# Optimization experiments

Measured on AMD Instinct MI355X. Metric: run time of the kernel, lower is better.

## Reference

```python
import jax, jax.numpy as jnp
import numpy as np

HEADS = 8
DIM_HEAD = 64
SCALE = DIM_HEAD ** -0.5


def setup_inputs() -> dict:
    key = jax.random.key(0)
    ks = jax.random.split(key, 6)
    b, n, t, d, cond_dim, hidden = 2, 8, 1024, 512, 512, HEADS * DIM_HEAD
    return {
        "x": jax.random.normal(ks[0], (b * n, t, d), dtype=jnp.float32),
        "label_emb_mm": jax.random.normal(ks[1], (b, n, cond_dim), dtype=jnp.float32),
        "Wqkv": jax.random.normal(ks[2], (d, 3 * hidden), dtype=jnp.float32) * (d ** -0.5),
        "Wk": jax.random.normal(ks[3], (cond_dim, hidden), dtype=jnp.float32) * (cond_dim ** -0.5),
        "Wv": jax.random.normal(ks[4], (cond_dim, hidden), dtype=jnp.float32) * (cond_dim ** -0.5),
        "Wout": jax.random.normal(ks[5], (hidden, d), dtype=jnp.float32) * (hidden ** -0.5),
        "b": 2,
    }


def reference(x, label_emb_mm, Wqkv, Wk, Wv, Wout, b):
    bn, t, d = x.shape
    n = bn // b
    h, dh = HEADS, DIM_HEAD
    xb = x.reshape(b, n, t, d)
    # fused QKV projection: (b, n, t, 3*h*dh)
    qkv = xb @ Wqkv
    q, k, v = jnp.split(qkv, 3, axis=-1)

    def to_heads(z):  # (b, n, t, h*dh) -> (b, n, h, t, dh)
        return z.reshape(b, n, t, h, dh).transpose(0, 1, 3, 2, 4)

    q, k, v = to_heads(q), to_heads(k), to_heads(v)
    # per-frame conditioning K/V: one extra token per frame
    ek = (label_emb_mm @ Wk).reshape(b, n, 1, h, dh).transpose(0, 1, 3, 2, 4)
    ev = (label_emb_mm @ Wv).reshape(b, n, 1, h, dh).transpose(0, 1, 3, 2, 4)
    k = jnp.concatenate([ek, k], axis=-2)  # (b, n, h, 1+t, dh)
    v = jnp.concatenate([ev, v], axis=-2)
    q = q * SCALE
    sim = jnp.einsum("bnhid,bnhjd->bnhij", q, k)
    attn = jax.nn.softmax(sim, axis=-1)
    out = jnp.einsum("bnhij,bnhjd->bnhid", attn, v)
    out = out.transpose(0, 1, 3, 2, 4).reshape(b, n, t, h * dh)
    out = out @ Wout
    return out.reshape(b * n, t, d)
```

## Files before the change

kernel.cpp:

```cpp
#include <hip/hip_runtime.h>
#include <stdint.h>

typedef unsigned short u16;
typedef __bf16 bf16x8 __attribute__((ext_vector_type(8)));
typedef float f32x4 __attribute__((ext_vector_type(4)));
typedef float f32x16 __attribute__((ext_vector_type(16)));

__device__ __forceinline__ u16 f2bf(float f) {
  uint32_t u = __builtin_bit_cast(uint32_t, f);
  u += 0x7FFFu + ((u >> 16) & 1u);
  return (u16)(u >> 16);
}
__device__ __forceinline__ float bf2f(u16 v) {
  return __builtin_bit_cast(float, ((uint32_t)v) << 16);
}

#if __has_builtin(__builtin_amdgcn_exp2f)
__device__ __forceinline__ float exp2_fast(float x) { return __builtin_amdgcn_exp2f(x); }
#else
__device__ __forceinline__ float exp2_fast(float x) { return exp2f(x); }
#endif

__device__ __forceinline__ void gload_lds16(const u16* g, u16* l) {
  __builtin_amdgcn_global_load_lds(
      (const __attribute__((address_space(1))) uint32_t*)g,
      (__attribute__((address_space(3))) uint32_t*)l, 16, 0, 0);
}

__device__ __forceinline__ uint32_t cvtpk(float lo, float hi) {
  uint32_t r;
  asm("v_cvt_pk_bf16_f32 %0, %1, %2" : "=v"(r) : "v"(lo), "v"(hi));
  return r;
}
__device__ __forceinline__ void plswap(uint32_t& a, uint32_t& b) {
  asm volatile("v_permlane32_swap_b32 %0, %1" : "+v"(a), "+v"(b));
}

__global__ __launch_bounds__(256) void prep_kernel(
    const float* __restrict__ x, const float* __restrict__ Wqkv,
    const float* __restrict__ Wout, const float* __restrict__ label,
    const float* __restrict__ Wk, const float* __restrict__ Wv,
    u16* __restrict__ xb, u16* __restrict__ WqkvT, u16* __restrict__ WoutT,
    u16* __restrict__ ek, u16* __restrict__ ev, float qscale) {
  const int b = blockIdx.x;
  if (b < 4096) {
    int i = (b * 256 + threadIdx.x) * 8;
    float4 a = *(const float4*)(x + i);
    float4 c = *(const float4*)(x + i + 4);
    union { u16 u[8]; uint4 v; } r;
    r.u[0] = f2bf(a.x); r.u[1] = f2bf(a.y); r.u[2] = f2bf(a.z); r.u[3] = f2bf(a.w);
    r.u[4] = f2bf(c.x); r.u[5] = f2bf(c.y); r.u[6] = f2bf(c.z); r.u[7] = f2bf(c.w);
    *(uint4*)(xb + i) = r.v;
  } else if (b < 7168) {
    int id = (b - 4096) * 256 + threadIdx.x;
    int k = id & 511, nn = id >> 9;
    float v = Wqkv[(size_t)k * 1536 + nn];
    if (nn < 512) v *= qscale;
    WqkvT[id] = f2bf(v);
  } else if (b < 8192) {
    int id = (b - 7168) * 256 + threadIdx.x;
    int k = id & 511, nn = id >> 9;
    WoutT[id] = f2bf(Wout[(size_t)k * 512 + nn]);
  } else {
    __shared__ float sdata[256];
    const int bb = b - 8192;
    const int chunk = bb & 7, row = (bb >> 3) & 15;
    const float* W = (bb & 128) ? Wv : Wk;
    u16* o = (bb & 128) ? ev : ek;
    const int tid = threadIdx.x;
    const int col = chunk * 64 + (tid & 63);
    const int ks = tid >> 6;
    const float* lr = label + row * 512 + ks * 128;
    const float* wp = W + (size_t)(ks * 128) * 512 + col;
    float acc = 0.f;
#pragma unroll 8
    for (int i = 0; i < 128; ++i)
      acc = fmaf(lr[i], wp[(size_t)i * 512], acc);
    sdata[tid] = acc;
    __syncthreads();
    if (tid < 64) {
      float t = sdata[tid] + sdata[tid + 64] + sdata[tid + 128] + sdata[tid + 192];
      o[row * 512 + chunk * 64 + tid] = f2bf(t);
    }
  }
}

template <int MODE>
__global__ __launch_bounds__(512, 2) void gemm_bt_kernel(
    const u16* __restrict__ A, const u16* __restrict__ B,
    u16* __restrict__ OQ, u16* __restrict__ OKb, u16* __restrict__ OVT,
    float* __restrict__ OF, int K, int N) {
  __shared__ __align__(16) u16 As[3][128 * 64];
  __shared__ __align__(16) u16 Bs[3][256 * 64];
  const int tid = threadIdx.x;
  const int w = tid >> 6, lane = tid & 63;
  const int l15 = lane & 15, lg = lane >> 4;
  const int wr = w >> 2, wc = w & 3;

  constexpr int NBY = (MODE == 0) ? 6 : 2;
  const int q8 = gridDim.x >> 3;
  const int cf = blockIdx.x;
  const int wg = (cf & 7) * q8 + (cf >> 3);
  const int bx = wg / NBY, by = wg % NBY;

  const int srow = tid >> 3, schunk = tid & 7;
  const u16* Ag = A + (size_t)(bx * 128 + srow) * K + ((schunk ^ (srow & 7)) * 8);
  const u16* Bg = B + (size_t)(by * 256 + srow) * K + ((schunk ^ (srow & 7)) * 8);

  f32x4 acc[4][4] = {};

  const int nt = K >> 6;
#define STAGE(buf, k0)                                                      \
  {                                                                         \
    gload_lds16(Ag + (k0), &As[buf][(w * 8) * 64]);                         \
    gload_lds16(Ag + (k0) + (size_t)64 * K, &As[buf][(64 + w * 8) * 64]);   \
    _Pragma("unroll") for (int r = 0; r < 4; ++r)                           \
        gload_lds16(Bg + (k0) + (size_t)(r * 64) * K,                       \
                    &Bs[buf][(r * 64 + w * 8) * 64]);                       \
  }
#define COMPUTE(cb)                                                               \
  {                                                                               \
    const u16* Ab = &As[cb][0];                                                   \
    const u16* Bb = &Bs[cb][0];                                                   \
    bf16x8 a[4][2], b[4][2];                                                      \
    _Pragma("unroll") for (int mi = 0; mi < 4; ++mi) {                            \
      const int row = wr * 64 + mi * 16 + l15;                                    \
      _Pragma("unroll") for (int ks = 0; ks < 2; ++ks)                            \
          a[mi][ks] = *(const bf16x8*)&Ab[row * 64 + (((ks * 4 + lg) ^ (row & 7)) * 8)]; \
    }                                                                             \
    _Pragma("unroll") for (int ni = 0; ni < 4; ++ni) {                            \
      const int row = wc * 64 + ni * 16 + l15;                                    \
      _Pragma("unroll") for (int ks = 0; ks < 2; ++ks)                            \
          b[ni][ks] = *(const bf16x8*)&Bb[row * 64 + (((ks * 4 + lg) ^ (row & 7)) * 8)]; \
    }                                                                             \
    __builtin_amdgcn_s_setprio(1);                                                \
    _Pragma("unroll") for (int ks = 0; ks < 2; ++ks)                              \
        _Pragma("unroll") for (int mi = 0; mi < 4; ++mi)                          \
            _Pragma("unroll") for (int ni = 0; ni < 4; ++ni)                      \
                acc[mi][ni] = __builtin_amdgcn_mfma_f32_16x16x32_bf16(             \
                    a[mi][ks], b[ni][ks], acc[mi][ni], 0, 0, 0);                  \
    __builtin_amdgcn_s_setprio(0);                                                \
  }

  STAGE(0, 0);
  STAGE(1, 64);

  int cr = 0, cw = 2;
  for (int t = 0; t < nt - 1; ++t) {
    asm volatile("s_waitcnt vmcnt(6)" ::: "memory");
    __builtin_amdgcn_s_barrier();
    __builtin_amdgcn_sched_barrier(0);
    if (t + 2 < nt) STAGE(cw, (t + 2) * 64);
    COMPUTE(cr);
    cr = (cr == 2) ? 0 : cr + 1;
    cw = (cw == 2) ? 0 : cw + 1;
  }
  asm volatile("s_waitcnt vmcnt(0)" ::: "memory");
  __builtin_amdgcn_s_barrier();
  __builtin_amdgcn_sched_barrier(0);
  COMPUTE(cr);
#undef STAGE
#undef COMPUTE

  const int row0 = bx * 128 + wr * 64 + lg * 4;
  if constexpr (MODE == 1) {
#pragma unroll
    for (int mi = 0; mi < 4; ++mi)
#pragma unroll
      for (int ni = 0; ni < 4; ++ni) {
        int col = by * 256 + wc * 64 + ni * 16 + l15;
#pragma unroll
        for (int r = 0; r < 4; ++r)
          OF[(size_t)(row0 + mi * 16 + r) * N + col] = acc[mi][ni][r];
      }
  } else {
#pragma unroll
    for (int mi = 0; mi < 4; ++mi)
#pragma unroll
      for (int ni = 0; ni < 4; ++ni) {
        const int gcol = by * 256 + wc * 64 + ni * 16 + l15;
        const int sect = gcol >> 9;
        const int colL = gcol & 511;
        if (sect < 2) {
          u16* O = sect ? OKb : OQ;
#pragma unroll
          for (int r = 0; r < 4; ++r)
            O[(size_t)(row0 + mi * 16 + r) * 512 + colL] = f2bf(acc[mi][ni][r]);
        } else {
          int h = colL >> 6, dh = colL & 63;
          int rr = row0 + mi * 16;
          int bn = rr >> 10, t0 = rr & 1023;
          ushort4 pk;
          pk.x = f2bf(acc[mi][ni][0]);
          pk.y = f2bf(acc[mi][ni][1]);
          pk.z = f2bf(acc[mi][ni][2]);
          pk.w = f2bf(acc[mi][ni][3]);
          *(ushort4*)&OVT[(size_t)((bn * 8 + h) * 64 + dh) * 1024 + t0] = pk;
        }
      }
  }
}

__global__ __launch_bounds__(256, 2) void attn_kernel(
    const u16* __restrict__ Qb, const u16* __restrict__ Kb, const u16* __restrict__ VTb,
    const u16* __restrict__ ekb, const u16* __restrict__ evb, u16* __restrict__ Ob) {
  __shared__ __align__(16) u16 Kl[64 * 64];
  __shared__ __align__(16) u16 Vl[64 * 64];

  const int tid = threadIdx.x;
  const int w = tid >> 6, lane = tid & 63;
  const int l31 = lane & 31, hi = lane >> 5;
  const int lb = (blockIdx.x & 7) * 64 + (blockIdx.x >> 3);
  const int head = lb >> 2, qt = lb & 3;
  const int bn = head >> 3, h = head & 7;
  const int q0 = qt * 256 + w * 64;

  const int sr = tid >> 3, sj = tid & 7;
  const int sdst = (sj ^ (sr & 7)) * 8;
  const u16* KgA = Kb + (size_t)(bn * 1024 + sr) * 512 + h * 64 + sj * 8;
  const u16* VgA = VTb + (size_t)(head * 64 + sr) * 1024 + sj * 8;
  u16* KlD = &Kl[sr * 64 + sdst];
  u16* VlD = &Vl[sr * 64 + sdst];

  uint4 kp0, kp1, vp0, vp1;
  {
    kp0 = *(const uint4*)(KgA);
    kp1 = *(const uint4*)(KgA + (size_t)32 * 512);
    vp0 = *(const uint4*)(VgA);
    vp1 = *(const uint4*)(VgA + (size_t)32 * 1024);
  }

  bf16x8 qf[2][4];
#pragma unroll
  for (int qs = 0; qs < 2; ++qs)
#pragma unroll
    for (int c = 0; c < 4; ++c)
      qf[qs][c] = *(const bf16x8*)(Qb + (size_t)(bn * 1024 + q0 + qs * 32 + l31) * 512 +
                                   h * 64 + c * 16 + hi * 8);

  bf16x8 bones1;
  {
    union { u16 u[8]; bf16x8 v; } ob;
#pragma unroll
    for (int j = 0; j < 8; ++j) ob.u[j] = (u16)0x3F80;
    bones1 = ob.v;
  }

  f32x16 acc[2][2];
  f32x16 acc5[2];
  {
    float dot[2] = {0.f, 0.f};
#pragma unroll
    for (int c = 0; c < 4; ++c) {
      bf16x8 ekf = *(const bf16x8*)(ekb + bn * 512 + h * 64 + c * 16 + hi * 8);
#pragma unroll
      for (int qs = 0; qs < 2; ++qs)
#pragma unroll
        for (int j = 0; j < 8; ++j)
          dot[qs] += (float)qf[qs][c][j] * (float)ekf[j];
    }
    union { u16 u[8]; bf16x8 v; } pef[2], evf[2];
#pragma unroll
    for (int qs = 0; qs < 2; ++qs) {
      uint32_t a = __builtin_bit_cast(uint32_t, dot[qs]), b = a;
      plswap(a, b);
      float part = (lane < 32) ? __builtin_bit_cast(float, b) : __builtin_bit_cast(float, a);
      float pe = exp2_fast(dot[qs] + part);
#pragma unroll
      for (int j = 0; j < 8; ++j) pef[qs].u[j] = 0;
      if (hi == 0) pef[qs].u[0] = f2bf(pe);
    }
#pragma unroll
    for (int dt = 0; dt < 2; ++dt) {
#pragma unroll
      for (int j = 0; j < 8; ++j) evf[dt].u[j] = 0;
      if (hi == 0) evf[dt].u[0] = evb[bn * 512 + h * 64 + dt * 32 + l31];
    }
    f32x16 z = {};
#pragma unroll
    for (int qs = 0; qs < 2; ++qs) {
#pragma unroll
      for (int dt = 0; dt < 2; ++dt)
        acc[qs][dt] = __builtin_amdgcn_mfma_f32_32x32x16_bf16(pef[qs].v, evf[dt].v, z, 0, 0, 0);
      acc5[qs] = __builtin_amdgcn_mfma_f32_32x32x16_bf16(pef[qs].v, bones1, z, 0, 0, 0);
    }
  }

  for (int jt = 0; jt < 16; ++jt) {
    __syncthreads();
    *(uint4*)(KlD) = kp0;
    *(uint4*)(KlD + 32 * 64) = kp1;
    *(uint4*)(VlD) = vp0;
    *(uint4*)(VlD + 32 * 64) = vp1;
    __syncthreads();

    if (jt < 15) {
      const int j0 = (jt + 1) * 64;
      kp0 = *(const uint4*)(KgA + (size_t)j0 * 512);
      kp1 = *(const uint4*)(KgA + (size_t)(j0 + 32) * 512);
      vp0 = *(const uint4*)(VgA + j0);
      vp1 = *(const uint4*)(VgA + j0 + (size_t)32 * 1024);
    }

#pragma unroll
    for (int sub = 0; sub < 2; ++sub) {
      const int rk = sub * 32 + l31;
      bf16x8 kb[4];
#pragma unroll
      for (int c = 0; c < 4; ++c)
        kb[c] = *(const bf16x8*)&Kl[rk * 64 + (((c * 2 + hi) ^ (rk & 7)) * 8)];

      f32x16 s[2] = {};
#pragma unroll
      for (int qs = 0; qs < 2; ++qs)
#pragma unroll
        for (int c = 0; c < 4; ++c)
          s[qs] = __builtin_amdgcn_mfma_f32_32x32x16_bf16(kb[c], qf[qs][c], s[qs], 0, 0, 0);

      bf16x8 pa[2][2];
#pragma unroll
      for (int qs = 0; qs < 2; ++qs) {
        uint32_t wd[8];
#pragma unroll
        for (int i = 0; i < 8; ++i)
          wd[i] = cvtpk(exp2_fast(s[qs][2 * i]), exp2_fast(s[qs][2 * i + 1]));
        plswap(wd[0], wd[2]);
        plswap(wd[1], wd[3]);
        plswap(wd[4], wd[6]);
        plswap(wd[5], wd[7]);
        union { uint32_t w[4]; bf16x8 v; } f0, f1;
        f0.w[0] = wd[0]; f0.w[1] = wd[1]; f0.w[2] = wd[2]; f0.w[3] = wd[3];
        f1.w[0] = wd[4]; f1.w[1] = wd[5]; f1.w[2] = wd[6]; f1.w[3] = wd[7];
        pa[qs][0] = f0.v;
        pa[qs][1] = f1.v;
      }

#pragma unroll
      for (int dt = 0; dt < 2; ++dt) {
        const int rv = dt * 32 + l31;
#pragma unroll
        for (int ch = 0; ch < 2; ++ch) {
          bf16x8 vb = *(const bf16x8*)&Vl[rv * 64 + (((sub * 4 + ch * 2 + hi) ^ (rv & 7)) * 8)];
#pragma unroll
          for (int qs = 0; qs < 2; ++qs)
            acc[qs][dt] = __builtin_amdgcn_mfma_f32_32x32x16_bf16(pa[qs][ch], vb, acc[qs][dt], 0, 0, 0);
        }
      }
#pragma unroll
      for (int qs = 0; qs < 2; ++qs)
#pragma unroll
        for (int ch = 0; ch < 2; ++ch)
          acc5[qs] = __builtin_amdgcn_mfma_f32_32x32x16_bf16(pa[qs][ch], bones1, acc5[qs], 0, 0, 0);
    }
  }

#pragma unroll
  for (int qs = 0; qs < 2; ++qs)
#pragma unroll
    for (int r = 0; r < 16; ++r) {
      const float inv = 1.0f / acc5[qs][r];
      const int q = q0 + qs * 32 + (r & 3) + 8 * (r >> 2) + 4 * hi;
      u16* op = Ob + (size_t)(bn * 1024 + q) * 512 + h * 64 + l31;
      op[0] = f2bf(acc[qs][0][r] * inv);
      op[32] = f2bf(acc[qs][1][r] * inv);
    }
}

extern "C" void kernel_launch(void* const* d_in, const int* in_sizes, int n_in,
                              void* d_out, int out_size, void* d_ws, size_t ws_size,
                              hipStream_t stream) {
  (void)in_sizes; (void)n_in; (void)out_size; (void)ws_size;
  const float* x     = (const float*)d_in[0];
  const float* label = (const float*)d_in[1];
  const float* Wqkv  = (const float*)d_in[2];
  const float* Wk    = (const float*)d_in[3];
  const float* Wv    = (const float*)d_in[4];
  const float* Wout  = (const float*)d_in[5];
  float* out = (float*)d_out;

  char* ws = (char*)d_ws;
  u16* xb    = (u16*)(ws);
  u16* WqkvT = (u16*)(ws + 16777216);
  u16* WoutT = (u16*)(ws + 18350080);
  u16* ekb   = (u16*)(ws + 18874368);
  u16* evb   = (u16*)(ws + 18890752);
  u16* Qbuf  = (u16*)(ws + 18907136);
  u16* Kbuf  = (u16*)(ws + 35684352);
  u16* VTbuf = (u16*)(ws + 52461568);

  const float qscale = 0.125f * 1.4426950408889634f;

  prep_kernel<<<8448, 256, 0, stream>>>(x, Wqkv, Wout, label, Wk, Wv,
                                        xb, WqkvT, WoutT, ekb, evb, qscale);

  gemm_bt_kernel<0><<<768, 512, 0, stream>>>(xb, WqkvT, Qbuf, Kbuf, VTbuf, nullptr, 512, 1536);

  attn_kernel<<<512, 256, 0, stream>>>(Qbuf, Kbuf, VTbuf, ekb, evb, xb);

  gemm_bt_kernel<1><<<256, 512, 0, stream>>>(xb, WoutT, nullptr, nullptr, nullptr, out, 512, 512);
}
```

Before: 122.4 us.

## Retile projection GEMMs to 256-row tiles with double buffering and precomputed LDS offsets

The GEMM kernel moves from 128x256 tiles with a three-buffer LDS ring to 256xBN tiles (BN=192 for the QKV projection, 128 for the output projection) with two LDS buffers. Each wave now holds 8xNI accumulators. The next tile's load is issued after compute behind an extra barrier, and swizzled LDS offsets are precomputed once outside the loop. The QKV launch drops from 768 to 512 blocks, and the output projection keeps 256 blocks. This raises A-operand reuse and cuts address math, at the cost of more register pressure, less load/compute overlap, an extra barrier per iteration, and fewer blocks per CU.

```diff
diff --git a/kernel.cpp b/kernel.cpp
--- a/kernel.cpp
+++ b/kernel.cpp
@@ -90,95 +90,116 @@
     const u16* __restrict__ A, const u16* __restrict__ B,
     u16* __restrict__ OQ, u16* __restrict__ OKb, u16* __restrict__ OVT,
     float* __restrict__ OF, int K, int N) {
-  __shared__ __align__(16) u16 As[3][128 * 64];
-  __shared__ __align__(16) u16 Bs[3][256 * 64];
+  constexpr int BN = (MODE == 0) ? 192 : 128;
+  constexpr int NI = BN / 64;
+  constexpr int NRB = BN / 64;
+  constexpr int NBY = (MODE == 0) ? 8 : 4;
+  constexpr int VM = 4 + NRB;
+
+  __shared__ __align__(16) u16 As[2][256 * 64];
+  __shared__ __align__(16) u16 Bs[2][BN * 64];
+
   const int tid = threadIdx.x;
   const int w = tid >> 6, lane = tid & 63;
   const int l15 = lane & 15, lg = lane >> 4;
   const int wr = w >> 2, wc = w & 3;
 
-  constexpr int NBY = (MODE == 0) ? 6 : 2;
   const int q8 = gridDim.x >> 3;
-  const int cf = blockIdx.x;
-  const int wg = (cf & 7) * q8 + (cf >> 3);
+  const int wg = (blockIdx.x & 7) * q8 + (blockIdx.x >> 3);
   const int bx = wg / NBY, by = wg % NBY;
 
   const int srow = tid >> 3, schunk = tid & 7;
-  const u16* Ag = A + (size_t)(bx * 128 + srow) * K + ((schunk ^ (srow & 7)) * 8);
-  const u16* Bg = B + (size_t)(by * 256 + srow) * K + ((schunk ^ (srow & 7)) * 8);
-
-  f32x4 acc[4][4] = {};
+  const u16* Ag = A + (size_t)(bx * 256 + srow) * K + ((schunk ^ (srow & 7)) * 8);
+  const u16* Bg = B + (size_t)(by * BN + srow) * K + ((schunk ^ (srow & 7)) * 8);
+
+  int aoff[8][2], boff[NI][2];
+#pragma unroll
+  for (int mi = 0; mi < 8; ++mi)
+#pragma unroll
+    for (int ks = 0; ks < 2; ++ks) {
+      const int row = wr * 128 + mi * 16 + l15;
+      aoff[mi][ks] = row * 64 + (((ks * 4 + lg) ^ (row & 7)) * 8);
+    }
+#pragma unroll
+  for (int ni = 0; ni < NI; ++ni)
+#pragma unroll
+    for (int ks = 0; ks < 2; ++ks) {
+      const int row = wc * (BN / 4) + ni * 16 + l15;
+      boff[ni][ks] = row * 64 + (((ks * 4 + lg) ^ (row & 7)) * 8);
+    }
+
+  f32x4 acc[8][NI] = {};
 
   const int nt = K >> 6;
-#define STAGE(buf, k0)                                                      \
-  {                                                                         \
-    gload_lds16(Ag + (k0), &As[buf][(w * 8) * 64]);                         \
-    gload_lds16(Ag + (k0) + (size_t)64 * K, &As[buf][(64 + w * 8) * 64]);   \
-    _Pragma("unroll") for (int r = 0; r < 4; ++r)                           \
-        gload_lds16(Bg + (k0) + (size_t)(r * 64) * K,                       \
-                    &Bs[buf][(r * 64 + w * 8) * 64]);                       \
-  }
-#define COMPUTE(cb)                                                               \
-  {                                                                               \
-    const u16* Ab = &As[cb][0];                                                   \
-    const u16* Bb = &Bs[cb][0];                                                   \
-    bf16x8 a[4][2], b[4][2];                                                      \
-    _Pragma("unroll") for (int mi = 0; mi < 4; ++mi) {                            \
-      const int row = wr * 64 + mi * 16 + l15;                                    \
-      _Pragma("unroll") for (int ks = 0; ks < 2; ++ks)                            \
-          a[mi][ks] = *(const bf16x8*)&Ab[row * 64 + (((ks * 4 + lg) ^ (row & 7)) * 8)]; \
-    }                                                                             \
-    _Pragma("unroll") for (int ni = 0; ni < 4; ++ni) {                            \
-      const int row = wc * 64 + ni * 16 + l15;                                    \
-      _Pragma("unroll") for (int ks = 0; ks < 2; ++ks)                            \
-          b[ni][ks] = *(const bf16x8*)&Bb[row * 64 + (((ks * 4 + lg) ^ (row & 7)) * 8)]; \
-    }                                                                             \
-    __builtin_amdgcn_s_setprio(1);                                                \
-    _Pragma("unroll") for (int ks = 0; ks < 2; ++ks)                              \
-        _Pragma("unroll") for (int mi = 0; mi < 4; ++mi)                          \
-            _Pragma("unroll") for (int ni = 0; ni < 4; ++ni)                      \
-                acc[mi][ni] = __builtin_amdgcn_mfma_f32_16x16x32_bf16(             \
-                    a[mi][ks], b[ni][ks], acc[mi][ni], 0, 0, 0);                  \
-    __builtin_amdgcn_s_setprio(0);                                                \
+#define STAGE(buf, k0)                                                       \
+  {                                                                          \
+    _Pragma("unroll") for (int ra = 0; ra < 4; ++ra)                         \
+        gload_lds16(Ag + (k0) + (size_t)(ra * 64) * K,                       \
+                    &As[buf][(ra * 64 + w * 8) * 64]);                       \
+    _Pragma("unroll") for (int rb = 0; rb < NRB; ++rb)                       \
+        gload_lds16(Bg + (k0) + (size_t)(rb * 64) * K,                       \
+                    &Bs[buf][(rb * 64 + w * 8) * 64]);                       \
+  }
+#define COMPUTE(cb)                                                          \
+  {                                                                          \
+    const u16* Ab = &As[cb][0];                                              \
+    const u16* Bb = &Bs[cb][0];                                              \
+    _Pragma("unroll") for (int ks = 0; ks < 2; ++ks) {                       \
+      bf16x8 a[8], b[NI];                                                    \
+      _Pragma("unroll") for (int mi = 0; mi < 8; ++mi)                       \
+          a[mi] = *(const bf16x8*)&Ab[aoff[mi][ks]];                         \
+      _Pragma("unroll") for (int ni = 0; ni < NI; ++ni)                      \
+          b[ni] = *(const bf16x8*)&Bb[boff[ni][ks]];                         \
+      __builtin_amdgcn_s_setprio(1);                                         \
+      _Pragma("unroll") for (int mi = 0; mi < 8; ++mi)                       \
+          _Pragma("unroll") for (int ni = 0; ni < NI; ++ni)                  \
+              acc[mi][ni] = __builtin_amdgcn_mfma_f32_16x16x32_bf16(          \
+                  a[mi], b[ni], acc[mi][ni], 0, 0, 0);                       \
+      __builtin_amdgcn_s_setprio(0);                                         \
+    }                                                                        \
   }
 
   STAGE(0, 0);
   STAGE(1, 64);
 
-  int cr = 0, cw = 2;
   for (int t = 0; t < nt - 1; ++t) {
-    asm volatile("s_waitcnt vmcnt(6)" ::: "memory");
+    if constexpr (VM == 7)
+      asm volatile("s_waitcnt vmcnt(7)" ::: "memory");
+    else
+      asm volatile("s_waitcnt vmcnt(6)" ::: "memory");
     __builtin_amdgcn_s_barrier();
     __builtin_amdgcn_sched_barrier(0);
-    if (t + 2 < nt) STAGE(cw, (t + 2) * 64);
-    COMPUTE(cr);
-    cr = (cr == 2) ? 0 : cr + 1;
-    cw = (cw == 2) ? 0 : cw + 1;
+    COMPUTE(t & 1);
+    if (t + 2 < nt) {
+      __builtin_amdgcn_s_barrier();
+      __builtin_amdgcn_sched_barrier(0);
+      STAGE(t & 1, (t + 2) * 64);
+    }
   }
   asm volatile("s_waitcnt vmcnt(0)" ::: "memory");
   __builtin_amdgcn_s_barrier();
   __builtin_amdgcn_sched_barrier(0);
-  COMPUTE(cr);
+  COMPUTE((nt - 1) & 1);
 #undef STAGE
 #undef COMPUTE
 
-  const int row0 = bx * 128 + wr * 64 + lg * 4;
+  const int row0 = bx * 256 + wr * 128 + lg * 4;
   if constexpr (MODE == 1) {
 #pragma unroll
-    for (int mi = 0; mi < 4; ++mi)
-#pragma unroll
-      for (int ni = 0; ni < 4; ++ni) {
-        int col = by * 256 + wc * 64 + ni * 16 + l15;
+    for (int mi = 0; mi < 8; ++mi)
+#pragma unroll
+      for (int ni = 0; ni < NI; ++ni) {
+        int col = by * BN + wc * (BN / 4) + ni * 16 + l15;
 #pragma unroll
         for (int r = 0; r < 4; ++r)
           OF[(size_t)(row0 + mi * 16 + r) * N + col] = acc[mi][ni][r];
       }
   } else {
 #pragma unroll
-    for (int mi = 0; mi < 4; ++mi)
-#pragma unroll
-      for (int ni = 0; ni < 4; ++ni) {
-        const int gcol = by * 256 + wc * 64 + ni * 16 + l15;
+    for (int mi = 0; mi < 8; ++mi)
+#pragma unroll
+      for (int ni = 0; ni < NI; ++ni) {
+        const int gcol = by * BN + wc * (BN / 4) + ni * 16 + l15;
         const int sect = gcol >> 9;
         const int colL = gcol & 511;
         if (sect < 2) {
@@ -393,7 +414,7 @@
   prep_kernel<<<8448, 256, 0, stream>>>(x, Wqkv, Wout, label, Wk, Wv,
                                         xb, WqkvT, WoutT, ekb, evb, qscale);
 
-  gemm_bt_kernel<0><<<768, 512, 0, stream>>>(xb, WqkvT, Qbuf, Kbuf, VTbuf, nullptr, 512, 1536);
+  gemm_bt_kernel<0><<<512, 512, 0, stream>>>(xb, WqkvT, Qbuf, Kbuf, VTbuf, nullptr, 512, 1536);
 
   attn_kernel<<<512, 256, 0, stream>>>(Qbuf, Kbuf, VTbuf, ekb, evb, xb);
 
```

After: 120.2 us. Within noise of the previous version (-1.8%).
